# Kernel tuning notes

Hardware: AMD Instinct MI355X
Metric: run time of the kernel (lower is better)

The kernel has to match this reference:

```python
import jax, jax.numpy as jnp
import numpy as np

UNITS = 256
GROUPS = 8
EPS = 1e-3  # keras GroupNormalization default epsilon


def group_norm(x, gamma, beta, groups=GROUPS, eps=EPS):
    # x: [B,H,W,C], normalize per group over (H,W,C//groups)
    B, H, W, C = x.shape
    xg = x.reshape(B, H, W, groups, C // groups)
    mean = xg.mean(axis=(1, 2, 4), keepdims=True)
    var = xg.var(axis=(1, 2, 4), keepdims=True)
    xn = (xg - mean) * jax.lax.rsqrt(var + eps)
    xn = xn.reshape(B, H, W, C)
    return xn * gamma + beta


def setup_inputs() -> dict:
    key = jax.random.key(0)
    ks = jax.random.split(key, 10)
    B, H, W, C = 4, 64, 64, UNITS
    s = 1.0 / np.sqrt(C)
    x = jax.random.normal(ks[0], (B, H, W, C), dtype=jnp.float32)
    return {
        "x": x,
        "gamma": jnp.ones((C,), jnp.float32),
        "beta": jnp.zeros((C,), jnp.float32),
        "Wq": jax.random.uniform(ks[1], (C, C), jnp.float32, -s, s),
        "bq": jnp.zeros((C,), jnp.float32),
        "Wk": jax.random.uniform(ks[2], (C, C), jnp.float32, -s, s),
        "bk": jnp.zeros((C,), jnp.float32),
        "Wv": jax.random.uniform(ks[3], (C, C), jnp.float32, -s, s),
        "bv": jnp.zeros((C,), jnp.float32),
        # proj kernel init scale ~0 -> near-zero weights; use tiny random for nontrivial grads
        "Wp": jax.random.uniform(ks[4], (C, C), jnp.float32, -1e-5, 1e-5),
        "bp": jnp.zeros((C,), jnp.float32),
    }


def reference(x, gamma, beta, Wq, bq, Wk, bk, Wv, bv, Wp, bp):
    B, H, W, C = x.shape
    scale = jnp.float32(C) ** -0.5
    xn = group_norm(x, gamma, beta)  # [B,H,W,C]
    n = H * W
    xf = xn.reshape(B, n, C)
    q = xf @ Wq + bq  # [B,N,C]
    k = xf @ Wk + bk
    v = xf @ Wv + bv
    attn = jnp.einsum('bnc,bmc->bnm', q, k) * scale  # [B,N,N]
    attn = jax.nn.softmax(attn, axis=-1)
    out = jnp.einsum('bnm,bmc->bnc', attn, v)  # [B,N,C]
    out = out @ Wp + bp
    # NOTE: original code reassigns `inputs = self.norm(inputs)` before the
    # residual, so the skip connection uses the NORMALIZED input.
    return xn + out.reshape(B, H, W, C)
```

## Files before the change

kernel.cpp:

```cpp
#include <hip/hip_runtime.h>
#include <hip/hip_bf16.h>

typedef unsigned short u16;
typedef unsigned char u8;
typedef short short8 __attribute__((ext_vector_type(8)));
typedef float floatx4 __attribute__((ext_vector_type(4)));
typedef int intx8 __attribute__((ext_vector_type(8)));
typedef long long i64;

#define BB 4
#define NN 4096
#define CC 256
#define NG 8
#define M_TOT (BB * NN)
#define GN_EPS 1e-3f
#define ATT_SCALE 0.0625f
#define MCONST 2.5f
#define UNIT_SCALE 0x7F7F7F7F

__device__ __forceinline__ u16 f2bf(float f) {
  __hip_bfloat16 h = __float2bfloat16(f);
  return __builtin_bit_cast(u16, h);
}
__device__ __forceinline__ float bf2f(u16 u) {
  unsigned int i = ((unsigned int)u) << 16;
  return __builtin_bit_cast(float, i);
}
__device__ __forceinline__ unsigned pack2(float a, float b) {
  return (unsigned)f2bf(a) | ((unsigned)f2bf(b) << 16);
}
__device__ __forceinline__ unsigned pk4f8(float a, float b, float c, float d) {
  unsigned v = __builtin_amdgcn_cvt_pk_fp8_f32(a, b, 0, false);
  v = __builtin_amdgcn_cvt_pk_fp8_f32(c, d, v, true);
  return v;
}
__device__ __forceinline__ u8 f8byte(float a) {
  return (u8)(__builtin_amdgcn_cvt_pk_fp8_f32(a, a, 0, false) & 0xFF);
}

typedef __attribute__((address_space(3))) unsigned int lds_u32;
typedef const __attribute__((address_space(1))) unsigned int glb_u32;
#define ASYNC16(g, l) \
  __builtin_amdgcn_global_load_lds((glb_u32*)(g), (lds_u32*)(l), 16, 0, 0)

__global__ void prep_stats(const float* __restrict__ x,
                           const float* __restrict__ Wq, const float* __restrict__ Wk,
                           const float* __restrict__ Wv, const float* __restrict__ Wp,
                           float* __restrict__ part,
                           u16* __restrict__ wqT, u16* __restrict__ wkT,
                           u16* __restrict__ wvT, u16* __restrict__ wpT) {
  __shared__ u16 Ts[64][68];
  int blk = blockIdx.x;
  int t = threadIdx.x;
  if (blk < 512) {
    int b = blk >> 7, chunk = blk & 127;
    const float* p = x + ((size_t)b * NN + chunk * 32) * CC + t;
    float s = 0.f, ss = 0.f;
    for (int i = 0; i < 32; ++i) { float v = p[(size_t)i * CC]; s += v; ss += v * v; }
    for (int off = 1; off < 32; off <<= 1) { s += __shfl_xor(s, off); ss += __shfl_xor(ss, off); }
    if ((t & 31) == 0) {
      int g = t >> 5;
      part[((size_t)blk * NG + g) * 2 + 0] = s;
      part[((size_t)blk * NG + g) * 2 + 1] = ss;
    }
  } else {
    int pid = blk - 512;
    int y = pid >> 4, tile = pid & 15;
    int o0 = (tile >> 2) * 64, c0 = (tile & 3) * 64;
    const float* W = (y == 0) ? Wq : (y == 1) ? Wk : (y == 2) ? Wv : Wp;
    u16* WT = (y == 0) ? wqT : (y == 1) ? wkT : (y == 2) ? wvT : wpT;
    int cl = t >> 4, o4 = t & 15;
    for (int it = 0; it < 4; ++it) {
      int c = cl + it * 16;
      float4 v = *reinterpret_cast<const float4*>(W + (size_t)(c0 + c) * CC + o0 + o4 * 4);
      Ts[c][o4 * 4 + 0] = f2bf(v.x); Ts[c][o4 * 4 + 1] = f2bf(v.y);
      Ts[c][o4 * 4 + 2] = f2bf(v.z); Ts[c][o4 * 4 + 3] = f2bf(v.w);
    }
    __syncthreads();
    int ol = t >> 3, c8 = t & 7;
    for (int it = 0; it < 2; ++it) {
      int o = ol + it * 32;
      uint4 uv;
      uv.x = (unsigned)Ts[c8 * 8 + 0][o] | ((unsigned)Ts[c8 * 8 + 1][o] << 16);
      uv.y = (unsigned)Ts[c8 * 8 + 2][o] | ((unsigned)Ts[c8 * 8 + 3][o] << 16);
      uv.z = (unsigned)Ts[c8 * 8 + 4][o] | ((unsigned)Ts[c8 * 8 + 5][o] << 16);
      uv.w = (unsigned)Ts[c8 * 8 + 6][o] | ((unsigned)Ts[c8 * 8 + 7][o] << 16);
      *reinterpret_cast<uint4*>(WT + (size_t)(o0 + o) * CC + c0 + c8 * 8) = uv;
    }
  }
}

__global__ __launch_bounds__(256) void gn_apply(
    const float* __restrict__ x, const float* __restrict__ gamma,
    const float* __restrict__ beta, const float* __restrict__ part,
    u16* __restrict__ xnb) {
  __shared__ float gnst[16];
  int blk = blockIdx.x;
  int t = threadIdx.x;
  int b = blk >> 7;
  if (t < 64) {
    int g = t >> 3, j = t & 7;
    float s = 0.f, ss = 0.f;
    for (int ch = j; ch < 128; ch += 8) {
      size_t idx = (((size_t)(b * 128 + ch)) * NG + g) * 2;
      s += part[idx]; ss += part[idx + 1];
    }
    for (int off = 1; off < 8; off <<= 1) { s += __shfl_xor(s, off); ss += __shfl_xor(ss, off); }
    if (j == 0) {
      const float cnt = (float)(NN * (CC / NG));
      float mean = s / cnt;
      float var = ss / cnt - mean * mean;
      gnst[g * 2] = mean;
      gnst[g * 2 + 1] = rsqrtf(var + GN_EPS);
    }
  }
  __syncthreads();
  int row0 = blk * 32;
#pragma unroll
  for (int it = 0; it < 8; ++it) {
    int idx = t + it * 256;
    int rl = idx >> 6, c4 = idx & 63;
    int g = c4 >> 3;
    float mean = gnst[g * 2], rstd = gnst[g * 2 + 1];
    size_t gidx = (size_t)(row0 + rl) * 64 + c4;
    float4 v = reinterpret_cast<const float4*>(x)[gidx];
    float4 gm = reinterpret_cast<const float4*>(gamma)[c4];
    float4 bt = reinterpret_cast<const float4*>(beta)[c4];
    ushort4 o;
    o.x = f2bf((v.x - mean) * rstd * gm.x + bt.x);
    o.y = f2bf((v.y - mean) * rstd * gm.y + bt.y);
    o.z = f2bf((v.z - mean) * rstd * gm.z + bt.z);
    o.w = f2bf((v.w - mean) * rstd * gm.w + bt.w);
    reinterpret_cast<ushort4*>(xnb)[gidx] = o;
  }
}

#define LDT 72
__global__ __launch_bounds__(256) void gemm_qkv(
    const u16* __restrict__ xnb,
    const u16* __restrict__ wqT, const u16* __restrict__ wkT, const u16* __restrict__ wvT,
    const float* __restrict__ bq, const float* __restrict__ bk, const float* __restrict__ bv,
    u8* __restrict__ qb, u8* __restrict__ kb, u8* __restrict__ vTb) {
  __shared__ u16 sm[2 * 128 * LDT];
  u16* Asp = sm;
  u16* Bsp = sm + 128 * LDT;
  int m0 = blockIdx.x * 128;
  int widx = blockIdx.y >> 1;
  int n0 = (blockIdx.y & 1) * 128;
  const u16* wT = (widx == 0) ? wqT : (widx == 1) ? wkT : wvT;
  const float* bias = (widx == 0) ? bq : (widx == 1) ? bk : bv;
  int t = threadIdx.x, w = t >> 6, lane = t & 63, lo = lane & 15, hi = lane >> 4;
  int wm = (w >> 1) * 64, wn = (w & 1) * 64;
  floatx4 acc[4][4];
  for (int i = 0; i < 4; ++i) for (int j = 0; j < 4; ++j) acc[i][j] = (floatx4){0.f, 0.f, 0.f, 0.f};
  for (int kt = 0; kt < 4; ++kt) {
    int k0 = kt * 64;
    __syncthreads();
    for (int i = 0; i < 4; ++i) {
      int idx = t + i * 256, r = idx >> 3, c8 = idx & 7;
      *reinterpret_cast<uint4*>(Asp + r * LDT + c8 * 8) =
          *reinterpret_cast<const uint4*>(xnb + (size_t)(m0 + r) * CC + k0 + c8 * 8);
      *reinterpret_cast<uint4*>(Bsp + r * LDT + c8 * 8) =
          *reinterpret_cast<const uint4*>(wT + (size_t)(n0 + r) * CC + k0 + c8 * 8);
    }
    __syncthreads();
    for (int k32 = 0; k32 < 2; ++k32) {
      short8 af[4], bfr[4];
      for (int mt = 0; mt < 4; ++mt)
        af[mt] = *reinterpret_cast<const short8*>(Asp + (wm + mt * 16 + lo) * LDT + k32 * 32 + hi * 8);
      for (int nt = 0; nt < 4; ++nt)
        bfr[nt] = *reinterpret_cast<const short8*>(Bsp + (wn + nt * 16 + lo) * LDT + k32 * 32 + hi * 8);
      for (int mt = 0; mt < 4; ++mt)
        for (int nt = 0; nt < 4; ++nt)
          acc[mt][nt] = __builtin_amdgcn_mfma_f32_16x16x32_bf16(af[mt], bfr[nt], acc[mt][nt], 0, 0, 0);
    }
  }
  __syncthreads();
  for (int mt = 0; mt < 4; ++mt)
    for (int nt = 0; nt < 4; ++nt)
      for (int r = 0; r < 4; ++r) {
        int rr = wm + mt * 16 + hi * 4 + r;
        int cc2 = wn + nt * 16 + lo;
        sm[rr * 130 + cc2] = f2bf(acc[mt][nt][r] + bias[n0 + cc2]);
      }
  __syncthreads();
  if (widx < 2) {
    u8* outp = (widx == 0) ? qb : kb;
    for (int j = 0; j < 8; ++j) {
      int c = t + j * 256;
      int row = c >> 4, chl = c & 15;
      const u16* sp = sm + row * 130 + chl * 8;
      uint2 val;
      val.x = pk4f8(bf2f(sp[0]), bf2f(sp[1]), bf2f(sp[2]), bf2f(sp[3]));
      val.y = pk4f8(bf2f(sp[4]), bf2f(sp[5]), bf2f(sp[6]), bf2f(sp[7]));
      int rowg = m0 + row;
      int chg = (n0 >> 3) + chl;
      *reinterpret_cast<uint2*>(outp + (size_t)rowg * CC + chg * 8) = val;
    }
  } else {
    int dloc = t & 127;
    int dglob = n0 + dloc;
    int bb = m0 >> 12, tk = m0 & (NN - 1);
    u8* dst = vTb + ((size_t)(bb * CC + dglob)) * NN + tk;
#pragma unroll
    for (int it = 0; it < 2; ++it) {
      int ub = (t >> 7) * 2 + it * 4;
      unsigned wds[8];
#pragma unroll
      for (int uo = 0; uo < 2; ++uo) {
        int u = ub + uo;
        int rbase = 64 * (u & 1) + 4 * (u >> 1);
#pragma unroll
        for (int q = 0; q < 4; ++q) {
          int r0 = rbase + q * 16;
          wds[uo * 4 + q] = pk4f8(bf2f(sm[(r0 + 0) * 130 + dloc]), bf2f(sm[(r0 + 1) * 130 + dloc]),
                                  bf2f(sm[(r0 + 2) * 130 + dloc]), bf2f(sm[(r0 + 3) * 130 + dloc]));
        }
      }
      *reinterpret_cast<uint4*>(dst + ub * 16) = (uint4){wds[0], wds[1], wds[2], wds[3]};
      *reinterpret_cast<uint4*>(dst + ub * 16 + 16) = (uint4){wds[4], wds[5], wds[6], wds[7]};
    }
  }
}

__global__ __launch_bounds__(256, 1) void fa_kernel(
    const u8* __restrict__ qb, const u8* __restrict__ kb, const u8* __restrict__ vTb,
    u8* __restrict__ Opart, float* __restrict__ Lpart, u16* __restrict__ aob, int S) {
  __shared__ u8 smem[131072];
  int by = blockIdx.y;
  int b = by / S, split = by - b * S;
  int t = threadIdx.x, w = t >> 6, lane = t & 63, lo = lane & 15, hi = lane >> 4;
  int qw = blockIdx.x * 128 + w * 32;

  const u8* kb_b = kb + (size_t)b * NN * CC;
  const u8* vb_b = vTb + (size_t)b * CC * NN;
  const int TILES = NN / 128;
  int jt0 = split * (TILES / S), jt1 = jt0 + TILES / S;

  int koffE = ((w << 5) + hi) * CC + ((lo ^ hi) << 4);
  int koffO = ((w << 5) + 4 + hi) * CC + ((lo ^ hi ^ 4) << 4);
  int voff  = ((w << 6) + (lane >> 3)) * NN + ((((lane & 7) ^ ((lane >> 3) & 7))) << 4);
  int ldsb  = (w * 512) * 16;

  auto STAGE = [&](u8* Kd, u8* Vd, int j0) {
    const u8* ksrc = kb_b + (size_t)j0 * CC;
    const u8* vsrc = vb_b + j0 + voff;
#pragma unroll
    for (int i2 = 0; i2 < 4; ++i2) {
      ASYNC16(ksrc + koffE + i2 * 2048, Kd + ldsb + (2 * i2) * 1024);
      ASYNC16(ksrc + koffO + i2 * 2048, Kd + ldsb + (2 * i2 + 1) * 1024);
    }
#pragma unroll
    for (int i = 0; i < 8; ++i)
      ASYNC16(vsrc + i * 32768, Vd + ldsb + i * 1024);
  };

  u8* Ka = smem;
  u8* Kn = smem + 32768;
  u8* Va = smem + 65536;
  u8* Vn = smem + 98304;

  STAGE(Ka, Va, jt0 * 128);

  intx8 qf[2][2];
#pragma unroll
  for (int qg = 0; qg < 2; ++qg) {
    const u8* qrow = qb + ((size_t)(b * NN + qw + qg * 16 + lo)) * CC;
#pragma unroll
    for (int kk = 0; kk < 2; ++kk) {
      uint4 a0 = *reinterpret_cast<const uint4*>(qrow + kk * 128 + hi * 32);
      uint4 a1 = *reinterpret_cast<const uint4*>(qrow + kk * 128 + hi * 32 + 16);
      qf[qg][kk] = (intx8){(int)a0.x, (int)a0.y, (int)a0.z, (int)a0.w,
                           (int)a1.x, (int)a1.y, (int)a1.z, (int)a1.w};
    }
  }
  floatx4 oacc[2][16];
#pragma unroll
  for (int qg = 0; qg < 2; ++qg)
#pragma unroll
    for (int dt = 0; dt < 16; ++dt) oacc[qg][dt] = (floatx4){0.f, 0.f, 0.f, 0.f};
  float lacc[2] = {0.f, 0.f};

  auto COMPUTE = [&](const u8* Kp, const u8* Vp) {
    int pAw[2][8];
#pragma unroll
    for (int g = 0; g < 8; ++g) {
      int row = g * 16 + lo;
      const u8* kr = Kp + row * 256;
      int rs = row & 7;
      floatx4 s0 = (floatx4){0.f, 0.f, 0.f, 0.f};
      floatx4 s1 = (floatx4){0.f, 0.f, 0.f, 0.f};
#pragma unroll
      for (int kk = 0; kk < 2; ++kk) {
        uint4 c0 = *reinterpret_cast<const uint4*>(kr + ((kk * 8 + hi * 2 + 0) ^ rs) * 16);
        uint4 c1 = *reinterpret_cast<const uint4*>(kr + ((kk * 8 + hi * 2 + 1) ^ rs) * 16);
        intx8 kf = (intx8){(int)c0.x, (int)c0.y, (int)c0.z, (int)c0.w,
                           (int)c1.x, (int)c1.y, (int)c1.z, (int)c1.w};
        s0 = __builtin_amdgcn_mfma_scale_f32_16x16x128_f8f6f4(
            kf, qf[0][kk], s0, 0, 0, 0, UNIT_SCALE, 0, UNIT_SCALE);
        s1 = __builtin_amdgcn_mfma_scale_f32_16x16x128_f8f6f4(
            kf, qf[1][kk], s1, 0, 0, 0, UNIT_SCALE, 0, UNIT_SCALE);
      }
      {
        float p0 = __expf(fmaf(s0[0], ATT_SCALE, -MCONST));
        float p1 = __expf(fmaf(s0[1], ATT_SCALE, -MCONST));
        float p2 = __expf(fmaf(s0[2], ATT_SCALE, -MCONST));
        float p3 = __expf(fmaf(s0[3], ATT_SCALE, -MCONST));
        lacc[0] += (p0 + p1) + (p2 + p3);
        pAw[0][g] = (int)pk4f8(p0, p1, p2, p3);
      }
      {
        float p0 = __expf(fmaf(s1[0], ATT_SCALE, -MCONST));
        float p1 = __expf(fmaf(s1[1], ATT_SCALE, -MCONST));
        float p2 = __expf(fmaf(s1[2], ATT_SCALE, -MCONST));
        float p3 = __expf(fmaf(s1[3], ATT_SCALE, -MCONST));
        lacc[1] += (p0 + p1) + (p2 + p3);
        pAw[1][g] = (int)pk4f8(p0, p1, p2, p3);
      }
    }
    intx8 pA0 = (intx8){pAw[0][0], pAw[0][1], pAw[0][2], pAw[0][3],
                        pAw[0][4], pAw[0][5], pAw[0][6], pAw[0][7]};
    intx8 pA1 = (intx8){pAw[1][0], pAw[1][1], pAw[1][2], pAw[1][3],
                        pAw[1][4], pAw[1][5], pAw[1][6], pAw[1][7]};

#pragma unroll
    for (int dt = 0; dt < 16; ++dt) {
      int d = dt * 16 + lo;
      const u8* vr = Vp + d * 128;
      int ds7 = d & 7;
      uint4 v0 = *reinterpret_cast<const uint4*>(vr + ((hi * 2 + 0) ^ ds7) * 16);
      uint4 v1 = *reinterpret_cast<const uint4*>(vr + ((hi * 2 + 1) ^ ds7) * 16);
      intx8 vf = (intx8){(int)v0.x, (int)v0.y, (int)v0.z, (int)v0.w,
                         (int)v1.x, (int)v1.y, (int)v1.z, (int)v1.w};
      oacc[0][dt] = __builtin_amdgcn_mfma_scale_f32_16x16x128_f8f6f4(
          pA0, vf, oacc[0][dt], 0, 0, 0, UNIT_SCALE, 0, UNIT_SCALE);
      oacc[1][dt] = __builtin_amdgcn_mfma_scale_f32_16x16x128_f8f6f4(
          pA1, vf, oacc[1][dt], 0, 0, 0, UNIT_SCALE, 0, UNIT_SCALE);
    }
  };

  __syncthreads();
  for (int jt = jt0; jt < jt1; ++jt) {
    if (jt + 1 < jt1) STAGE(Kn, Vn, (jt + 1) * 128);
    COMPUTE(Ka, Va);
    __syncthreads();
    u8* tk = Ka; Ka = Kn; Kn = tk;
    u8* tv = Va; Va = Vn; Vn = tv;
  }

#pragma unroll
  for (int qg = 0; qg < 2; ++qg) {
    lacc[qg] += __shfl_xor(lacc[qg], 16);
    lacc[qg] += __shfl_xor(lacc[qg], 32);
  }

  if (S == 1) {
#pragma unroll
    for (int qg = 0; qg < 2; ++qg) {
      float inv[4];
#pragma unroll
      for (int r = 0; r < 4; ++r) inv[r] = 1.0f / __shfl(lacc[qg], 4 * hi + r);
#pragma unroll
      for (int dt = 0; dt < 16; ++dt)
#pragma unroll
        for (int r = 0; r < 4; ++r) {
          size_t row = (size_t)(b * NN + qw + qg * 16 + 4 * hi + r);
          aob[row * CC + dt * 16 + lo] = f2bf(oacc[qg][dt][r] * inv[r]);
        }
    }
  } else {
    if (hi == 0) {
#pragma unroll
      for (int qg = 0; qg < 2; ++qg)
        Lpart[(size_t)split * M_TOT + b * NN + qw + qg * 16 + lo] = lacc[qg];
    }
    u8* op = Opart + (size_t)split * M_TOT * CC;
#pragma unroll
    for (int qg = 0; qg < 2; ++qg)
#pragma unroll
      for (int dt = 0; dt < 16; ++dt)
#pragma unroll
        for (int r = 0; r < 4; ++r) {
          size_t row = (size_t)(b * NN + qw + qg * 16 + 4 * hi + r);
          op[row * CC + dt * 16 + lo] = f8byte(oacc[qg][dt][r]);
        }
  }
}

__global__ __launch_bounds__(256) void gemm_proj(
    const u16* __restrict__ aob, const u8* __restrict__ Opart,
    const float* __restrict__ Lpart,
    const u16* __restrict__ wpT, const float* __restrict__ bp,
    const u16* __restrict__ xnb, float* __restrict__ out, int S) {
  __shared__ u16 As[64 * LDT];
  __shared__ u16 Bs[128 * LDT];
  __shared__ float linv[64];
  int m0 = blockIdx.x * 64;
  int n0 = blockIdx.y * 128;
  int t = threadIdx.x, w = t >> 6, lane = t & 63, lo = lane & 15, hi = lane >> 4;
  int wm = (w >> 1) * 32, wn = (w & 1) * 64;
  if (S > 1 && t < 64) {
    float l = 0.f;
    for (int sp = 0; sp < S; ++sp) l += Lpart[(size_t)sp * M_TOT + m0 + t];
    linv[t] = 1.f / l;
  }
  floatx4 acc[2][4];
  for (int i = 0; i < 2; ++i) for (int j = 0; j < 4; ++j) acc[i][j] = (floatx4){0.f, 0.f, 0.f, 0.f};
  for (int kt = 0; kt < 4; ++kt) {
    int k0 = kt * 64;
    __syncthreads();
    for (int i = 0; i < 2; ++i) {
      int c = t + i * 256, r = c >> 3, c8 = c & 7;
      if (S == 1) {
        *reinterpret_cast<uint4*>(As + r * LDT + c8 * 8) =
            *reinterpret_cast<const uint4*>(aob + (size_t)(m0 + r) * CC + k0 + c8 * 8);
      } else {
        float f[8] = {0, 0, 0, 0, 0, 0, 0, 0};
        for (int sp = 0; sp < S; ++sp) {
          uint2 uv = *reinterpret_cast<const uint2*>(
              Opart + (size_t)sp * M_TOT * CC + (size_t)(m0 + r) * CC + k0 + c8 * 8);
          f[0] += __builtin_amdgcn_cvt_f32_fp8(uv.x, 0);
          f[1] += __builtin_amdgcn_cvt_f32_fp8(uv.x, 1);
          f[2] += __builtin_amdgcn_cvt_f32_fp8(uv.x, 2);
          f[3] += __builtin_amdgcn_cvt_f32_fp8(uv.x, 3);
          f[4] += __builtin_amdgcn_cvt_f32_fp8(uv.y, 0);
          f[5] += __builtin_amdgcn_cvt_f32_fp8(uv.y, 1);
          f[6] += __builtin_amdgcn_cvt_f32_fp8(uv.y, 2);
          f[7] += __builtin_amdgcn_cvt_f32_fp8(uv.y, 3);
        }
        float iv = linv[r];
        uint4 o;
        o.x = pack2(f[0] * iv, f[1] * iv); o.y = pack2(f[2] * iv, f[3] * iv);
        o.z = pack2(f[4] * iv, f[5] * iv); o.w = pack2(f[6] * iv, f[7] * iv);
        *reinterpret_cast<uint4*>(As + r * LDT + c8 * 8) = o;
      }
    }
    for (int i = 0; i < 4; ++i) {
      int c = t + i * 256, r = c >> 3, c8 = c & 7;
      *reinterpret_cast<uint4*>(Bs + r * LDT + c8 * 8) =
          *reinterpret_cast<const uint4*>(wpT + (size_t)(n0 + r) * CC + k0 + c8 * 8);
    }
    __syncthreads();
    for (int k32 = 0; k32 < 2; ++k32) {
      short8 af[2], bfr[4];
      for (int mt = 0; mt < 2; ++mt)
        af[mt] = *reinterpret_cast<const short8*>(As + (wm + mt * 16 + lo) * LDT + k32 * 32 + hi * 8);
      for (int nt = 0; nt < 4; ++nt)
        bfr[nt] = *reinterpret_cast<const short8*>(Bs + (wn + nt * 16 + lo) * LDT + k32 * 32 + hi * 8);
      for (int mt = 0; mt < 2; ++mt)
        for (int nt = 0; nt < 4; ++nt)
          acc[mt][nt] = __builtin_amdgcn_mfma_f32_16x16x32_bf16(af[mt], bfr[nt], acc[mt][nt], 0, 0, 0);
    }
  }
  for (int mt = 0; mt < 2; ++mt)
    for (int nt = 0; nt < 4; ++nt)
      for (int r = 0; r < 4; ++r) {
        int row = m0 + wm + mt * 16 + hi * 4 + r;
        int col = n0 + wn + nt * 16 + lo;
        size_t o = (size_t)row * CC + col;
        out[o] = acc[mt][nt][r] + bp[col] + bf2f(xnb[o]);
      }
}

extern "C" void kernel_launch(void* const* d_in, const int* in_sizes, int n_in,
                              void* d_out, int out_size, void* d_ws, size_t ws_size,
                              hipStream_t stream) {
  (void)in_sizes; (void)n_in; (void)out_size;
  const float* x     = (const float*)d_in[0];
  const float* gamma = (const float*)d_in[1];
  const float* beta  = (const float*)d_in[2];
  const float* Wq    = (const float*)d_in[3];
  const float* bq    = (const float*)d_in[4];
  const float* Wk    = (const float*)d_in[5];
  const float* bk    = (const float*)d_in[6];
  const float* Wv    = (const float*)d_in[7];
  const float* bv    = (const float*)d_in[8];
  const float* Wp    = (const float*)d_in[9];
  const float* bp    = (const float*)d_in[10];
  float* out = (float*)d_out;

  char* w = (char*)d_ws;
  float* part  = (float*)w;              w += 512 * NG * 2 * 4;
  const size_t SZ = (size_t)M_TOT * CC * 2;
  const size_t SZ8 = (size_t)M_TOT * CC;
  u16* xnb = (u16*)w; w += SZ;
  u8* qb   = (u8*)w;  w += SZ8;
  u8* kb   = (u8*)w;  w += SZ8;
  u8* vTb  = (u8*)w;  w += SZ8;
  u16* aob = (u16*)w; w += SZ;
  u16* wqT = (u16*)w; w += (size_t)CC * CC * 2;
  u16* wkT = (u16*)w; w += (size_t)CC * CC * 2;
  u16* wvT = (u16*)w; w += (size_t)CC * CC * 2;
  u16* wpT = (u16*)w; w += (size_t)CC * CC * 2;

  size_t used = (size_t)(w - (char*)d_ws);
  size_t per_split = SZ8 + (size_t)M_TOT * 4 + 256;
  int S = 2;
  if (used + 2 * per_split > ws_size) S = 1;
  u8* Opart = (u8*)w;                    w += (size_t)S * SZ8;
  float* Lpart = (float*)w;

  prep_stats<<<576, 256, 0, stream>>>(x, Wq, Wk, Wv, Wp, part, wqT, wkT, wvT, wpT);
  gn_apply<<<512, 256, 0, stream>>>(x, gamma, beta, part, xnb);
  gemm_qkv<<<dim3(M_TOT / 128, 6), 256, 0, stream>>>(xnb, wqT, wkT, wvT, bq, bk, bv, qb, kb, vTb);
  fa_kernel<<<dim3(NN / 128, BB * S), 256, 0, stream>>>(qb, kb, vTb, Opart, Lpart, aob, S);
  gemm_proj<<<dim3(M_TOT / 64, 2), 256, 0, stream>>>(aob, Opart, Lpart, wpT, bp, xnb, out, S);
}
```

Baseline: 180.2 us.

## Pre-swizzle K/V global layout, widen FA blocks to 512 threads, raise split count

The QKV GEMM now writes K rows and transposed V with an XOR swizzle of each 16-byte chunk, keyed on row index, so the flash-attention kernel can stage tiles with plain linear async copies instead of computing per-lane swizzled addresses. The FA kernel moves to 512-thread blocks covering 256 queries each, with launch bounds asking for two blocks per CU, and the KV split count rises to 4 when workspace allows. Group-norm statistics switch to float4 loads with an LDS cross-wave reduction. The risks are register pressure under the new launch bounds, and 128 KB of shared memory per block may still allow only one block per CU. The extra splits also add partial-output traffic for the projection kernel to merge.

```diff
diff --git a/kernel.cpp b/kernel.cpp
--- a/kernel.cpp
+++ b/kernel.cpp
@@ -50,18 +50,29 @@
                            u16* __restrict__ wqT, u16* __restrict__ wkT,
                            u16* __restrict__ wvT, u16* __restrict__ wpT) {
   __shared__ u16 Ts[64][68];
+  __shared__ float red[4][8][2];
   int blk = blockIdx.x;
   int t = threadIdx.x;
   if (blk < 512) {
     int b = blk >> 7, chunk = blk & 127;
-    const float* p = x + ((size_t)b * NN + chunk * 32) * CC + t;
+    const float4* p4 = reinterpret_cast<const float4*>(
+        x + ((size_t)b * NN + chunk * 32) * CC);
+    int w = t >> 6, lane = t & 63;
     float s = 0.f, ss = 0.f;
-    for (int i = 0; i < 32; ++i) { float v = p[(size_t)i * CC]; s += v; ss += v * v; }
-    for (int off = 1; off < 32; off <<= 1) { s += __shfl_xor(s, off); ss += __shfl_xor(ss, off); }
-    if ((t & 31) == 0) {
-      int g = t >> 5;
-      part[((size_t)blk * NG + g) * 2 + 0] = s;
-      part[((size_t)blk * NG + g) * 2 + 1] = ss;
+#pragma unroll
+    for (int i = 0; i < 8; ++i) {
+      int r = w + i * 4;
+      float4 v = p4[r * 64 + lane];
+      s += (v.x + v.y) + (v.z + v.w);
+      ss += (v.x * v.x + v.y * v.y) + (v.z * v.z + v.w * v.w);
+    }
+    for (int off = 1; off < 8; off <<= 1) { s += __shfl_xor(s, off); ss += __shfl_xor(ss, off); }
+    if ((lane & 7) == 0) { red[w][lane >> 3][0] = s; red[w][lane >> 3][1] = ss; }
+    __syncthreads();
+    if (t < 16) {
+      int g = t >> 1, q = t & 1;
+      float a = red[0][g][q] + red[1][g][q] + red[2][g][q] + red[3][g][q];
+      part[((size_t)blk * NG + g) * 2 + q] = a;
     }
   } else {
     int pid = blk - 512;
@@ -195,11 +206,19 @@
       val.y = pk4f8(bf2f(sp[4]), bf2f(sp[5]), bf2f(sp[6]), bf2f(sp[7]));
       int rowg = m0 + row;
       int chg = (n0 >> 3) + chl;
-      *reinterpret_cast<uint2*>(outp + (size_t)rowg * CC + chg * 8) = val;
+      int pos;
+      if (widx == 0) {
+        pos = chg * 8;
+      } else {
+        int c16 = chg >> 1;
+        pos = (((c16 ^ (rowg & 7)) << 4)) + (chg & 1) * 8;
+      }
+      *reinterpret_cast<uint2*>(outp + (size_t)rowg * CC + pos) = val;
     }
   } else {
     int dloc = t & 127;
     int dglob = n0 + dloc;
+    int s7 = dglob & 7;
     int bb = m0 >> 12, tk = m0 & (NN - 1);
     u8* dst = vTb + ((size_t)(bb * CC + dglob)) * NN + tk;
 #pragma unroll
@@ -217,42 +236,37 @@
                                   bf2f(sm[(r0 + 2) * 130 + dloc]), bf2f(sm[(r0 + 3) * 130 + dloc]));
         }
       }
-      *reinterpret_cast<uint4*>(dst + ub * 16) = (uint4){wds[0], wds[1], wds[2], wds[3]};
-      *reinterpret_cast<uint4*>(dst + ub * 16 + 16) = (uint4){wds[4], wds[5], wds[6], wds[7]};
-    }
-  }
-}
-
-__global__ __launch_bounds__(256, 1) void fa_kernel(
+      *reinterpret_cast<uint4*>(dst + ((ub ^ s7) << 4)) = (uint4){wds[0], wds[1], wds[2], wds[3]};
+      *reinterpret_cast<uint4*>(dst + (((ub + 1) ^ s7) << 4)) = (uint4){wds[4], wds[5], wds[6], wds[7]};
+    }
+  }
+}
+
+__global__ __launch_bounds__(512, 2) void fa_kernel(
     const u8* __restrict__ qb, const u8* __restrict__ kb, const u8* __restrict__ vTb,
     u8* __restrict__ Opart, float* __restrict__ Lpart, u16* __restrict__ aob, int S) {
   __shared__ u8 smem[131072];
   int by = blockIdx.y;
   int b = by / S, split = by - b * S;
   int t = threadIdx.x, w = t >> 6, lane = t & 63, lo = lane & 15, hi = lane >> 4;
-  int qw = blockIdx.x * 128 + w * 32;
+  int qw = blockIdx.x * 256 + w * 32;
 
   const u8* kb_b = kb + (size_t)b * NN * CC;
   const u8* vb_b = vTb + (size_t)b * CC * NN;
   const int TILES = NN / 128;
   int jt0 = split * (TILES / S), jt1 = jt0 + TILES / S;
 
-  int koffE = ((w << 5) + hi) * CC + ((lo ^ hi) << 4);
-  int koffO = ((w << 5) + 4 + hi) * CC + ((lo ^ hi ^ 4) << 4);
-  int voff  = ((w << 6) + (lane >> 3)) * NN + ((((lane & 7) ^ ((lane >> 3) & 7))) << 4);
-  int ldsb  = (w * 512) * 16;
+  int vlaneoff = (lane >> 3) * NN + (lane & 7) * 16;
 
   auto STAGE = [&](u8* Kd, u8* Vd, int j0) {
-    const u8* ksrc = kb_b + (size_t)j0 * CC;
-    const u8* vsrc = vb_b + j0 + voff;
-#pragma unroll
-    for (int i2 = 0; i2 < 4; ++i2) {
-      ASYNC16(ksrc + koffE + i2 * 2048, Kd + ldsb + (2 * i2) * 1024);
-      ASYNC16(ksrc + koffO + i2 * 2048, Kd + ldsb + (2 * i2 + 1) * 1024);
-    }
-#pragma unroll
-    for (int i = 0; i < 8; ++i)
-      ASYNC16(vsrc + i * 32768, Vd + ldsb + i * 1024);
+    const u8* ksrc = kb_b + (size_t)j0 * CC + lane * 16;
+    const u8* vsrc = vb_b + j0 + (size_t)w * 8 * NN + vlaneoff;
+#pragma unroll
+    for (int i = 0; i < 4; ++i) {
+      int base = w * 64 + i * 512;
+      ASYNC16(ksrc + base * 16, Kd + base * 16);
+      ASYNC16(vsrc + (size_t)i * 64 * NN, Vd + base * 16);
+    }
   };
 
   u8* Ka = smem;
@@ -495,7 +509,8 @@
 
   size_t used = (size_t)(w - (char*)d_ws);
   size_t per_split = SZ8 + (size_t)M_TOT * 4 + 256;
-  int S = 2;
+  int S = 4;
+  if (used + 4 * per_split > ws_size) S = 2;
   if (used + 2 * per_split > ws_size) S = 1;
   u8* Opart = (u8*)w;                    w += (size_t)S * SZ8;
   float* Lpart = (float*)w;
@@ -503,6 +518,6 @@
   prep_stats<<<576, 256, 0, stream>>>(x, Wq, Wk, Wv, Wp, part, wqT, wkT, wvT, wpT);
   gn_apply<<<512, 256, 0, stream>>>(x, gamma, beta, part, xnb);
   gemm_qkv<<<dim3(M_TOT / 128, 6), 256, 0, stream>>>(xnb, wqT, wkT, wvT, bq, bk, bv, qb, kb, vTb);
-  fa_kernel<<<dim3(NN / 128, BB * S), 256, 0, stream>>>(qb, kb, vTb, Opart, Lpart, aob, S);
+  fa_kernel<<<dim3(NN / 256, BB * S), 512, 0, stream>>>(qb, kb, vTb, Opart, Lpart, aob, S);
   gemm_proj<<<dim3(M_TOT / 64, 2), 256, 0, stream>>>(aob, Opart, Lpart, wpT, bp, xnb, out, S);
 }
```

Result: slower. 184.3 us (+2.3%).
